# Kernel tuning notes

Hardware: AMD Instinct MI355X
Metric: run time of the kernel (lower is better)

## Reference

```python
import jax, jax.numpy as jnp
import numpy as np

B, T, D = 4, 2048, 1024
H = 16
DK = D // H

def setup_inputs() -> dict:
    key = jax.random.key(0)
    k1, k2, k3, k4, k5 = jax.random.split(key, 5)
    s = 1.0 / np.sqrt(D)
    return {
        "x": jax.random.normal(k1, (B, T, D), dtype=jnp.float32),
        # torch Linear convention: weight [out, in], y = x @ W.T + b
        "W_qkv": jax.random.uniform(k2, (3 * D, D), jnp.float32, -s, s),
        "b_qkv": jax.random.uniform(k3, (3 * D,), jnp.float32, -s, s),
        "W_proj": jax.random.uniform(k4, (D, D), jnp.float32, -s, s),
        "b_proj": jax.random.uniform(k5, (D,), jnp.float32, -s, s),
    }

def reference(x, W_qkv, b_qkv, W_proj, b_proj):
    Bx, Tx, C = x.shape
    qkv = x @ W_qkv.T + b_qkv                      # [B,T,3D]
    qkv = qkv.reshape(Bx, Tx, 3, H, DK)
    qkv = jnp.transpose(qkv, (2, 0, 3, 1, 4))      # [3,B,H,T,dk]
    q, k, v = qkv[0], qkv[1], qkv[2]
    att = jnp.einsum('bhqd,bhkd->bhqk', q, k) / np.sqrt(DK)
    causal = jnp.tril(jnp.ones((Tx, Tx), dtype=bool))
    att = jnp.where(causal[None, None], att, -jnp.inf)
    att = jax.nn.softmax(att, axis=-1)
    out = jnp.einsum('bhqk,bhkd->bhqd', att, v)    # [B,H,T,dk]
    out = jnp.transpose(out, (0, 2, 1, 3)).reshape(Bx, Tx, C)
    return out @ W_proj.T + b_proj
```

## Files before the change

kernel.cpp:

```cpp
#include <hip/hip_runtime.h>

typedef unsigned short ushort_t;
typedef __attribute__((ext_vector_type(8))) short short8;
typedef __attribute__((ext_vector_type(4))) float f32x4;

#define DEV __device__ __forceinline__

constexpr int B_ = 4, T_ = 2048, D_ = 1024, H_ = 16;
constexpr int M_ = B_ * T_;
constexpr float LOG2E_ = 1.4426950408889634f;

DEV ushort_t f2bf(float f) {
  union { float f; unsigned u; } c; c.f = f;
  unsigned u = c.u;
  return (ushort_t)((u + 0x7fffu + ((u >> 16) & 1u)) >> 16);
}
DEV float bf2f(ushort_t b) {
  union { unsigned u; float f; } c; c.u = ((unsigned)b) << 16;
  return c.f;
}
DEV unsigned cvt_pk_bf16(float lo, float hi) {
  unsigned r;
  asm("v_cvt_pk_bf16_f32 %0, %1, %2" : "=v"(r) : "v"(lo), "v"(hi));
  return r;
}

DEV void gload_lds16(const void* g, void* l) {
  __builtin_amdgcn_global_load_lds(
      (const __attribute__((address_space(1))) void*)g,
      (__attribute__((address_space(3))) void*)l, 16, 0, 0);
}

__global__ void __launch_bounds__(256) f2bf3_kernel(
    const float* __restrict__ a, ushort_t* __restrict__ oa, int na4,
    const float* __restrict__ b, ushort_t* __restrict__ ob, int nb4,
    const float* __restrict__ c, ushort_t* __restrict__ oc, int nc4) {
  int stride = gridDim.x * blockDim.x;
  int ntot = na4 + nb4 + nc4;
  for (int i = blockIdx.x * blockDim.x + threadIdx.x; i < ntot; i += stride) {
    const float* src;
    ushort_t* dst;
    int j = i;
    if (j < na4) {
      src = a; dst = oa;
    } else if (j < na4 + nb4) {
      j -= na4; src = b; dst = ob;
    } else {
      j -= na4 + nb4; src = c; dst = oc;
    }
    float4 v = reinterpret_cast<const float4*>(src)[j];
    ushort4 o;
    o.x = f2bf(v.x); o.y = f2bf(v.y); o.z = f2bf(v.z); o.w = f2bf(v.w);
    reinterpret_cast<ushort4*>(dst)[j] = o;
  }
}

template <bool OUT_BF16>
__global__ void __launch_bounds__(256) gemm_bt(
    const ushort_t* __restrict__ A, const ushort_t* __restrict__ Bw,
    const float* __restrict__ bias, void* __restrict__ Cout,
    ushort_t* __restrict__ VT, int M, int N, int K, int ldc) {
  __shared__ __align__(16) ushort_t lA[128 * 64];
  __shared__ __align__(16) ushort_t lB[128 * 64];
  const int tid = threadIdx.x;
  const int lane = tid & 63;
  const int w = tid >> 6;
  const int wm = w >> 1, wn = w & 1;
  const int r0 = lane & 15;
  const int g8 = (lane >> 4) * 8;

  const int gx = gridDim.x;
  const int lin = blockIdx.y * gx + blockIdx.x;
  const int cpx = (gx * gridDim.y) >> 3;
  const int swz = (lin & 7) * cpx + (lin >> 3);
  const int m0 = (swz / gx) * 128, n0 = (swz % gx) * 128;

  f32x4 acc[4][4] = {};

  for (int k0 = 0; k0 < K; k0 += 64) {
    int flat = tid * 8;
    for (int it = 0; it < 4; ++it) {
      int f = it * 2048 + flat;
      int row = f >> 6, col = f & 63;
      gload_lds16(A + (size_t)(m0 + row) * K + k0 + col, &lA[f]);
      gload_lds16(Bw + (size_t)(n0 + row) * K + k0 + col, &lB[f]);
    }
    __syncthreads();
    __builtin_amdgcn_s_setprio(1);
    for (int kc = 0; kc < 64; kc += 32) {
      short8 aF[4], bF[4];
      for (int mi = 0; mi < 4; ++mi)
        aF[mi] = *(const short8*)&lA[(wm * 64 + mi * 16 + r0) * 64 + kc + g8];
      for (int ni = 0; ni < 4; ++ni)
        bF[ni] = *(const short8*)&lB[(wn * 64 + ni * 16 + r0) * 64 + kc + g8];
      for (int mi = 0; mi < 4; ++mi)
        for (int ni = 0; ni < 4; ++ni)
          acc[mi][ni] = __builtin_amdgcn_mfma_f32_16x16x32_bf16(
              aF[mi], bF[ni], acc[mi][ni], 0, 0, 0);
    }
    __builtin_amdgcn_s_setprio(0);
    __syncthreads();
  }

  const int rg = (lane >> 4) * 4;
  const bool vpath = (VT != nullptr) && (n0 >= 2048);
  if (vpath) {
    for (int mi = 0; mi < 4; ++mi)
      for (int ni = 0; ni < 4; ++ni) {
        int n = n0 + wn * 64 + ni * 16 + r0;
        float bv = bias[n];
        int vcol = n - 2048;
        int hh = vcol >> 6, dd = vcol & 63;
        int m = m0 + wm * 64 + mi * 16 + rg;
        int bb = m >> 11, tt = m & 2047;
        ushort4 o;
        o.x = f2bf(acc[mi][ni][0] + bv);
        o.y = f2bf(acc[mi][ni][1] + bv);
        o.z = f2bf(acc[mi][ni][2] + bv);
        o.w = f2bf(acc[mi][ni][3] + bv);
        *reinterpret_cast<ushort4*>(
            &VT[((size_t)((bb << 4) + hh) * 64 + dd) * (size_t)T_ + tt]) = o;
      }
  } else {
    for (int mi = 0; mi < 4; ++mi)
      for (int ni = 0; ni < 4; ++ni) {
        int n = n0 + wn * 64 + ni * 16 + r0;
        float bv = bias[n];
        for (int r = 0; r < 4; ++r) {
          int m = m0 + wm * 64 + mi * 16 + rg + r;
          float v = acc[mi][ni][r] + bv;
          if (OUT_BF16)
            ((ushort_t*)Cout)[(size_t)m * ldc + n] = f2bf(v);
          else
            ((float*)Cout)[(size_t)m * ldc + n] = v;
        }
      }
  }
}

__global__ void __launch_bounds__(256, 4) attn_kernel(
    const ushort_t* __restrict__ qk, const ushort_t* __restrict__ Vt,
    ushort_t* __restrict__ O) {
  __shared__ __align__(16) ushort_t lK[2][64 * 64];
  __shared__ __align__(16) ushort_t lVT[2][64 * 64];
  __shared__ __align__(16) ushort_t lP[4][16 * 64];

  const int tid = threadIdx.x;
  const int lane = tid & 63;
  const int w = tid >> 6;
  const int r0 = lane & 15;
  const int p = lane >> 4;
  const int g8 = p * 8;
  const int rg = p * 4;

  const int lin = (int)blockIdx.y * 16 + (int)blockIdx.x;
  const int xcd = lin & 7;
  const int chunk = lin >> 3;
  const int bh = xcd * 8 + (chunk >> 4);
  const int pair = chunk & 15;

  const int b = bh >> 4, h = bh & 15;
  const float QSC = 0.125f * LOG2E_;

  const short8 bOne = {0x3F80, 0x3F80, 0x3F80, 0x3F80,
                       0x3F80, 0x3F80, 0x3F80, 0x3F80};

  ushort_t* lPw = &lP[w][0];

  const int f0 = tid * 8;
  const int row0 = f0 >> 6;
  const int lch0 = ((f0 >> 3) & 7) ^ (row0 & 7);
  const int f1 = 2048 + tid * 8;
  const int row1 = f1 >> 6;
  const int lch1 = ((f1 >> 3) & 7) ^ (row1 & 7);

  const int qb1 = pair;
  const int qb2 = 31 - pair;
  const int q1 = qb1 * 64 + w * 16;
  const int q2 = qb2 * 64 + w * 16;

  short8 aQ1[2], aQ2[2];
#pragma unroll
  for (int kc = 0; kc < 2; ++kc) {
    short8 raw1 = *(const short8*)(qk + (size_t)(b * T_ + q1 + r0) * 2048 +
                                   h * 64 + kc * 32 + g8);
    short8 raw2 = *(const short8*)(qk + (size_t)(b * T_ + q2 + r0) * 2048 +
                                   h * 64 + kc * 32 + g8);
    short8 s1, s2;
#pragma unroll
    for (int j = 0; j < 4; ++j) {
      unsigned pk1 = cvt_pk_bf16(bf2f((ushort_t)raw1[2 * j]) * QSC,
                                 bf2f((ushort_t)raw1[2 * j + 1]) * QSC);
      unsigned pk2 = cvt_pk_bf16(bf2f((ushort_t)raw2[2 * j]) * QSC,
                                 bf2f((ushort_t)raw2[2 * j + 1]) * QSC);
      s1[2 * j] = (short)(ushort_t)pk1;
      s1[2 * j + 1] = (short)(ushort_t)(pk1 >> 16);
      s2[2 * j] = (short)(ushort_t)pk2;
      s2[2 * j + 1] = (short)(ushort_t)(pk2 >> 16);
    }
    aQ1[kc] = s1;
    aQ2[kc] = s2;
  }

  f32x4 accO1[4] = {}, accO2[4] = {};
  f32x4 accL1 = {}, accL2 = {};

  {
    const ushort_t* kb = qk + (size_t)(b * T_) * 2048 + 1024 + h * 64;
    const ushort_t* vb = Vt + (size_t)bh * 64 * (size_t)T_;
    gload_lds16(kb + (size_t)row0 * 2048 + lch0 * 8, &lK[0][f0]);
    gload_lds16(kb + (size_t)row1 * 2048 + lch1 * 8, &lK[0][f1]);
    gload_lds16(vb + (size_t)row0 * T_ + lch0 * 8, &lVT[0][f0]);
    gload_lds16(vb + (size_t)row1 * T_ + lch1 * 8, &lVT[0][f1]);
  }
  int cur = 0;

  auto procPV = [&](f32x4* sA, const ushort_t* bufV, f32x4* accO,
                    f32x4& accL) {
#pragma unroll
    for (int ni = 0; ni < 4; ++ni) {
      float p0 = exp2f(sA[ni][0]);
      float p1 = exp2f(sA[ni][1]);
      float p2 = exp2f(sA[ni][2]);
      float p3 = exp2f(sA[ni][3]);
      unsigned lo = cvt_pk_bf16(p0, p1);
      unsigned hi = cvt_pk_bf16(p2, p3);
      int col = ni * 16 + r0;
#pragma unroll
      for (int r = 0; r < 4; ++r) {
        int rowp = rg + r;
        ushort_t hw = (r == 0)   ? (ushort_t)lo
                      : (r == 1) ? (ushort_t)(lo >> 16)
                      : (r == 2) ? (ushort_t)hi
                                 : (ushort_t)(hi >> 16);
        lPw[rowp * 64 + (col ^ ((rowp & 7) << 3))] = hw;
      }
    }
    __builtin_amdgcn_s_setprio(1);
#pragma unroll
    for (int kc = 0; kc < 2; ++kc) {
      int pch = (kc * 4 + p) ^ (r0 & 7);
      short8 aP = *(const short8*)&lPw[r0 * 64 + pch * 8];
      accL = __builtin_amdgcn_mfma_f32_16x16x32_bf16(aP, bOne, accL, 0, 0, 0);
#pragma unroll
      for (int ni = 0; ni < 4; ++ni) {
        int row = ni * 16 + r0;
        int ch = (kc * 4 + p) ^ (row & 7);
        short8 bV = *(const short8*)&bufV[row * 64 + ch * 8];
        accO[ni] =
            __builtin_amdgcn_mfma_f32_16x16x32_bf16(aP, bV, accO[ni], 0, 0, 0);
      }
    }
    __builtin_amdgcn_s_setprio(0);
  };

  for (int kt = 0; kt <= qb2; ++kt) {
    __syncthreads();

    if (kt < qb2) {
      const ushort_t* kb =
          qk + (size_t)(b * T_ + (kt + 1) * 64) * 2048 + 1024 + h * 64;
      const ushort_t* vb = Vt + (size_t)bh * 64 * (size_t)T_ + (kt + 1) * 64;
      ushort_t* dK = &lK[cur ^ 1][0];
      ushort_t* dV = &lVT[cur ^ 1][0];
      gload_lds16(kb + (size_t)row0 * 2048 + lch0 * 8, dK + f0);
      gload_lds16(kb + (size_t)row1 * 2048 + lch1 * 8, dK + f1);
      gload_lds16(vb + (size_t)row0 * T_ + lch0 * 8, dV + f0);
      gload_lds16(vb + (size_t)row1 * T_ + lch1 * 8, dV + f1);
    }

    const ushort_t* bufK = &lK[cur][0];
    const ushort_t* bufV = &lVT[cur][0];
    const bool act1 = (kt <= qb1);

    f32x4 sA2[4];
#pragma unroll
    for (int ni = 0; ni < 4; ++ni)
      sA2[ni] = f32x4{-16.f, -16.f, -16.f, -16.f};
    __builtin_amdgcn_s_setprio(1);
#pragma unroll
    for (int kc = 0; kc < 2; ++kc)
#pragma unroll
      for (int ni = 0; ni < 4; ++ni) {
        int row = ni * 16 + r0;
        int ch = (kc * 4 + p) ^ (row & 7);
        short8 bK = *(const short8*)&bufK[row * 64 + ch * 8];
        sA2[ni] =
            __builtin_amdgcn_mfma_f32_16x16x32_bf16(aQ2[kc], bK, sA2[ni], 0, 0, 0);
      }
    __builtin_amdgcn_s_setprio(0);
    if (kt == qb2) {
#pragma unroll
      for (int ni = 0; ni < 4; ++ni) {
        if (ni > w) {
#pragma unroll
          for (int r = 0; r < 4; ++r) sA2[ni][r] = -1e30f;
        } else if (ni == w) {
#pragma unroll
          for (int r = 0; r < 4; ++r)
            if (r0 > rg + r) sA2[ni][r] = -1e30f;
        }
      }
    }
    procPV(sA2, bufV, accO2, accL2);

    if (act1) {
      f32x4 sA1[4];
#pragma unroll
      for (int ni = 0; ni < 4; ++ni)
        sA1[ni] = f32x4{-16.f, -16.f, -16.f, -16.f};
      __builtin_amdgcn_s_setprio(1);
#pragma unroll
      for (int kc = 0; kc < 2; ++kc)
#pragma unroll
        for (int ni = 0; ni < 4; ++ni) {
          int row = ni * 16 + r0;
          int ch = (kc * 4 + p) ^ (row & 7);
          short8 bK = *(const short8*)&bufK[row * 64 + ch * 8];
          sA1[ni] = __builtin_amdgcn_mfma_f32_16x16x32_bf16(aQ1[kc], bK,
                                                            sA1[ni], 0, 0, 0);
        }
      __builtin_amdgcn_s_setprio(0);
      if (kt == qb1) {
#pragma unroll
        for (int ni = 0; ni < 4; ++ni) {
          if (ni > w) {
#pragma unroll
            for (int r = 0; r < 4; ++r) sA1[ni][r] = -1e30f;
          } else if (ni == w) {
#pragma unroll
            for (int r = 0; r < 4; ++r)
              if (r0 > rg + r) sA1[ni][r] = -1e30f;
          }
        }
      }
      procPV(sA1, bufV, accO1, accL1);
    }

    cur ^= 1;
  }

#pragma unroll
  for (int ni = 0; ni < 4; ++ni)
#pragma unroll
    for (int r = 0; r < 4; ++r) {
      int d = h * 64 + ni * 16 + r0;
      float v1 = accO1[ni][r] / accL1[r];
      float v2 = accO2[ni][r] / accL2[r];
      O[(size_t)(b * T_ + q1 + rg + r) * 1024 + d] = f2bf(v1);
      O[(size_t)(b * T_ + q2 + rg + r) * 1024 + d] = f2bf(v2);
    }
}

extern "C" void kernel_launch(void* const* d_in, const int* in_sizes, int n_in,
                              void* d_out, int out_size, void* d_ws, size_t ws_size,
                              hipStream_t stream) {
  const float* x = (const float*)d_in[0];
  const float* Wqkv = (const float*)d_in[1];
  const float* bqkv = (const float*)d_in[2];
  const float* Wproj = (const float*)d_in[3];
  const float* bproj = (const float*)d_in[4];
  float* out = (float*)d_out;

  ushort_t* xb = (ushort_t*)d_ws;
  ushort_t* wqkvb = xb + (size_t)M_ * D_;
  ushort_t* wprojb = wqkvb + (size_t)3 * D_ * D_;
  ushort_t* qkb = wprojb + (size_t)D_ * D_;
  ushort_t* Vt = qkb + (size_t)M_ * 2048;
  ushort_t* Ob = Vt + (size_t)M_ * D_;

  f2bf3_kernel<<<2048, 256, 0, stream>>>(
      x, xb, M_ * D_ / 4,
      Wqkv, wqkvb, 3 * D_ * D_ / 4,
      Wproj, wprojb, D_ * D_ / 4);

  gemm_bt<true><<<dim3(24, 64), 256, 0, stream>>>(
      xb, wqkvb, bqkv, qkb, Vt, M_, 3 * D_, D_, 2048);

  attn_kernel<<<dim3(16, 64), 256, 0, stream>>>(qkb, Vt, Ob);

  gemm_bt<false><<<dim3(8, 64), 256, 0, stream>>>(
      Ob, wprojb, bproj, out, nullptr, M_, D_, D_, D_);
}
```

Baseline: 195.4 us.

## Swizzle GEMM LDS layout and compute two N-tiles per block

Each GEMM block now computes two adjacent 128-column output tiles in sequence, which halves the grid size and is meant to reuse the A rows through cache. LDS tiles are stored with an XOR swizzle on 16-byte chunks so that the MFMA fragment reads avoid bank conflicts. The trade-off is fewer blocks for occupancy and tail balance, plus the A tile being reloaded from global memory for the second tile.

```diff
diff --git a/kernel.cpp b/kernel.cpp
--- a/kernel.cpp
+++ b/kernel.cpp
@@ -67,74 +67,95 @@
   const int w = tid >> 6;
   const int wm = w >> 1, wn = w & 1;
   const int r0 = lane & 15;
-  const int g8 = (lane >> 4) * 8;
-
-  const int gx = gridDim.x;
-  const int lin = blockIdx.y * gx + blockIdx.x;
-  const int cpx = (gx * gridDim.y) >> 3;
+  const int p = lane >> 4;
+  const int g8 = p * 8;
+  const int rg = p * 4;
+
+  const int tn2 = N >> 8;
+  const int G = (M >> 7) * tn2;
+  const int lin = blockIdx.x;
+  const int cpx = G >> 3;
   const int swz = (lin & 7) * cpx + (lin >> 3);
-  const int m0 = (swz / gx) * 128, n0 = (swz % gx) * 128;
-
-  f32x4 acc[4][4] = {};
-
-  for (int k0 = 0; k0 < K; k0 += 64) {
-    int flat = tid * 8;
-    for (int it = 0; it < 4; ++it) {
-      int f = it * 2048 + flat;
-      int row = f >> 6, col = f & 63;
-      gload_lds16(A + (size_t)(m0 + row) * K + k0 + col, &lA[f]);
-      gload_lds16(Bw + (size_t)(n0 + row) * K + k0 + col, &lB[f]);
-    }
-    __syncthreads();
-    __builtin_amdgcn_s_setprio(1);
-    for (int kc = 0; kc < 64; kc += 32) {
-      short8 aF[4], bF[4];
+  const int m0 = (swz / tn2) * 128;
+  const int pn = swz % tn2;
+
+  const int sf0 = tid * 8;
+
+  for (int t = 0; t < 2; ++t) {
+    const int n0 = (pn * 2 + t) * 128;
+
+    f32x4 acc[4][4] = {};
+
+    for (int k0 = 0; k0 < K; k0 += 64) {
+#pragma unroll
+      for (int it = 0; it < 4; ++it) {
+        int f = it * 2048 + sf0;
+        int row = f >> 6;
+        int lch = ((f >> 3) & 7) ^ (row & 7);
+        gload_lds16(A + (size_t)(m0 + row) * K + k0 + lch * 8, &lA[f]);
+        gload_lds16(Bw + (size_t)(n0 + row) * K + k0 + lch * 8, &lB[f]);
+      }
+      __syncthreads();
+      __builtin_amdgcn_s_setprio(1);
+#pragma unroll
+      for (int kc = 0; kc < 2; ++kc) {
+        const int ch = (kc * 4 + p) ^ (r0 & 7);
+        short8 aF[4], bF[4];
+#pragma unroll
+        for (int mi = 0; mi < 4; ++mi)
+          aF[mi] = *(const short8*)&lA[(wm * 64 + mi * 16 + r0) * 64 + ch * 8];
+#pragma unroll
+        for (int ni = 0; ni < 4; ++ni)
+          bF[ni] = *(const short8*)&lB[(wn * 64 + ni * 16 + r0) * 64 + ch * 8];
+#pragma unroll
+        for (int mi = 0; mi < 4; ++mi)
+#pragma unroll
+          for (int ni = 0; ni < 4; ++ni)
+            acc[mi][ni] = __builtin_amdgcn_mfma_f32_16x16x32_bf16(
+                aF[mi], bF[ni], acc[mi][ni], 0, 0, 0);
+      }
+      __builtin_amdgcn_s_setprio(0);
+      __syncthreads();
+    }
+
+    const bool vpath = (VT != nullptr) && (n0 >= 2048);
+    if (vpath) {
+#pragma unroll
       for (int mi = 0; mi < 4; ++mi)
-        aF[mi] = *(const short8*)&lA[(wm * 64 + mi * 16 + r0) * 64 + kc + g8];
-      for (int ni = 0; ni < 4; ++ni)
-        bF[ni] = *(const short8*)&lB[(wn * 64 + ni * 16 + r0) * 64 + kc + g8];
+#pragma unroll
+        for (int ni = 0; ni < 4; ++ni) {
+          int n = n0 + wn * 64 + ni * 16 + r0;
+          float bv = bias[n];
+          int vcol = n - 2048;
+          int hh = vcol >> 6, dd = vcol & 63;
+          int m = m0 + wm * 64 + mi * 16 + rg;
+          int bb = m >> 11, tt = m & 2047;
+          ushort4 o;
+          o.x = f2bf(acc[mi][ni][0] + bv);
+          o.y = f2bf(acc[mi][ni][1] + bv);
+          o.z = f2bf(acc[mi][ni][2] + bv);
+          o.w = f2bf(acc[mi][ni][3] + bv);
+          *reinterpret_cast<ushort4*>(
+              &VT[((size_t)((bb << 4) + hh) * 64 + dd) * (size_t)T_ + tt]) = o;
+        }
+    } else {
+#pragma unroll
       for (int mi = 0; mi < 4; ++mi)
-        for (int ni = 0; ni < 4; ++ni)
-          acc[mi][ni] = __builtin_amdgcn_mfma_f32_16x16x32_bf16(
-              aF[mi], bF[ni], acc[mi][ni], 0, 0, 0);
-    }
-    __builtin_amdgcn_s_setprio(0);
-    __syncthreads();
-  }
-
-  const int rg = (lane >> 4) * 4;
-  const bool vpath = (VT != nullptr) && (n0 >= 2048);
-  if (vpath) {
-    for (int mi = 0; mi < 4; ++mi)
-      for (int ni = 0; ni < 4; ++ni) {
-        int n = n0 + wn * 64 + ni * 16 + r0;
-        float bv = bias[n];
-        int vcol = n - 2048;
-        int hh = vcol >> 6, dd = vcol & 63;
-        int m = m0 + wm * 64 + mi * 16 + rg;
-        int bb = m >> 11, tt = m & 2047;
-        ushort4 o;
-        o.x = f2bf(acc[mi][ni][0] + bv);
-        o.y = f2bf(acc[mi][ni][1] + bv);
-        o.z = f2bf(acc[mi][ni][2] + bv);
-        o.w = f2bf(acc[mi][ni][3] + bv);
-        *reinterpret_cast<ushort4*>(
-            &VT[((size_t)((bb << 4) + hh) * 64 + dd) * (size_t)T_ + tt]) = o;
-      }
-  } else {
-    for (int mi = 0; mi < 4; ++mi)
-      for (int ni = 0; ni < 4; ++ni) {
-        int n = n0 + wn * 64 + ni * 16 + r0;
-        float bv = bias[n];
-        for (int r = 0; r < 4; ++r) {
-          int m = m0 + wm * 64 + mi * 16 + rg + r;
-          float v = acc[mi][ni][r] + bv;
-          if (OUT_BF16)
-            ((ushort_t*)Cout)[(size_t)m * ldc + n] = f2bf(v);
-          else
-            ((float*)Cout)[(size_t)m * ldc + n] = v;
+#pragma unroll
+        for (int ni = 0; ni < 4; ++ni) {
+          int n = n0 + wn * 64 + ni * 16 + r0;
+          float bv = bias[n];
+#pragma unroll
+          for (int r = 0; r < 4; ++r) {
+            int m = m0 + wm * 64 + mi * 16 + rg + r;
+            float v = acc[mi][ni][r] + bv;
+            if (OUT_BF16)
+              ((ushort_t*)Cout)[(size_t)m * ldc + n] = f2bf(v);
+            else
+              ((float*)Cout)[(size_t)m * ldc + n] = v;
+          }
         }
-      }
+    }
   }
 }
 
@@ -374,11 +395,11 @@
       Wqkv, wqkvb, 3 * D_ * D_ / 4,
       Wproj, wprojb, D_ * D_ / 4);
 
-  gemm_bt<true><<<dim3(24, 64), 256, 0, stream>>>(
+  gemm_bt<true><<<768, 256, 0, stream>>>(
       xb, wqkvb, bqkv, qkb, Vt, M_, 3 * D_, D_, 2048);
 
   attn_kernel<<<dim3(16, 64), 256, 0, stream>>>(qkb, Vt, Ob);
 
-  gemm_bt<false><<<dim3(8, 64), 256, 0, stream>>>(
+  gemm_bt<false><<<256, 256, 0, stream>>>(
       Ob, wprojb, bproj, out, nullptr, M_, D_, D_, D_);
 }
```

Result: no change. 196.7 us (+0.7%).
